# Performance work log

Hardware: AMD Instinct MI355X
Metric: run time of the kernel (lower is better)

## Reference

```python
import jax, jax.numpy as jnp
import numpy as np

NS = 16384  # number of samples
N = 2048    # number of sites


def setup_inputs() -> dict:
    key = jax.random.key(0)
    kx, kk = jax.random.split(key)
    x = jax.random.normal(kx, (NS, N), dtype=jnp.float32)
    kernel = 0.01 * jax.random.normal(kk, (N * (N - 1) // 2,), dtype=jnp.float32)
    return {"x": x, "kernel": kernel, "n": 4}


def reference(x, kernel, n):
    # Build strictly lower-triangular W from the kernel vector (sorted, unique indices)
    Nloc = x.shape[-1]
    il = jnp.tril_indices(Nloc, k=-1)
    W = jnp.zeros((Nloc, Nloc), dtype=kernel.dtype).at[il].set(
        kernel, unique_indices=True, indices_are_sorted=True)
    # z_nj = sum_i x_ni W_ji  ==  x @ W.T
    z = x @ W.T
    # each step: z_nk = sum_j z_nj W_kj x_nj  ==  (z * x) @ W.T
    z = jax.lax.fori_loop(0, n - 2, lambda i, zz: (zz * x) @ W.T, z)
    # logpsi_n = sum_l z_nl x_nl
    return jnp.sum(z * x, axis=-1)
```

## Files before the change

### kernel.cpp

```cpp
#include <hip/hip_runtime.h>
#include <stdint.h>

#define NSAMP 16384
#define NSITE 2048
#define BM 128
#define BN 128
#define BK 32
#define NT_M (NSAMP / BM)
#define NT_N (NSITE / BN)

typedef _Float16 f16x8 __attribute__((ext_vector_type(8)));
typedef float f32x16 __attribute__((ext_vector_type(16)));

__device__ __forceinline__ unsigned short f2h(float f) {
  _Float16 h = (_Float16)f;
  return __builtin_bit_cast(unsigned short, h);
}

__device__ __forceinline__ void gload_lds16(const void* g, void* l) {
  __builtin_amdgcn_global_load_lds(
      (const __attribute__((address_space(1))) void*)g,
      (__attribute__((address_space(3))) void*)l, 16, 0, 0);
}

#define SBAR() __builtin_amdgcn_sched_barrier(0)
#define BAR()  do { SBAR(); __builtin_amdgcn_s_barrier(); SBAR(); } while (0)
#define WLGKM(N) do { asm volatile("s_waitcnt lgkmcnt(" #N ")" ::: "memory"); SBAR(); } while (0)
#define WVM(N)   do { asm volatile("s_waitcnt vmcnt(" #N ")" ::: "memory"); SBAR(); } while (0)

__global__ void build_w_kernel(const float* __restrict__ kern,
                               unsigned short* __restrict__ W) {
  int idx = blockIdx.x * blockDim.x + threadIdx.x;
  int j = idx >> 11;
  int i = idx & (NSITE - 1);
  float v = 0.0f;
  if (i < j) v = kern[j * (j - 1) / 2 + i];
  W[idx] = f2h(v);
}

__global__ void build_x_kernel(const float* __restrict__ x,
                               unsigned short* __restrict__ X) {
  int idx = blockIdx.x * blockDim.x + threadIdx.x;
  const float4 v = reinterpret_cast<const float4*>(x)[idx];
  reinterpret_cast<ushort4*>(X)[idx] =
      make_ushort4(f2h(v.x), f2h(v.y), f2h(v.z), f2h(v.w));
}

template <int EPI>
__global__ __launch_bounds__(256, 3) void gemm_pass(
    const unsigned short* __restrict__ A, const unsigned short* __restrict__ W,
    const float* __restrict__ x, unsigned short* __restrict__ P,
    float* __restrict__ out) {
  __shared__ unsigned short lds[3][2][BM * BK];

  const int bid = blockIdx.x;
  const int g = bid >> 7;
  const int nt = (g & 1) ? (g >> 1) : (15 - (g >> 1));
  const int mt = bid & 127;
  const int m0 = mt * BM;
  const int n0 = nt * BN;

  const int tid = threadIdx.x;
  const int lane = tid & 63;
  const int wid = tid >> 6;
  const int wm = wid >> 1;
  const int wn = wid & 1;
  const int l32 = lane & 31;
  const int hi2 = lane >> 5;

  f32x16 acc[2][2] = {};
  f16x8 fa[2][2], fb[2][2];

  const int nkt = (n0 + BN) / BK;

  auto STAGE = [&](int kidx) {
    const int slot = kidx % 3;
#pragma unroll
    for (int inst = 0; inst < 4; ++inst) {
      const int p = inst >> 1;
      const int r = (inst & 1) * 64 + (tid >> 2);
      const int gch = (tid & 3) ^ ((r >> 1) & 3);
      const unsigned short* gp = p ? W : A;
      const int rb = p ? n0 : m0;
      const char* src =
          (const char*)(gp + (size_t)(rb + r) * NSITE + kidx * BK) + gch * 16;
      char* dst = (char*)&lds[slot][p][0] + (inst & 1) * 4096 + tid * 16;
      gload_lds16(src, dst);
    }
  };

  auto LDA_ = [&](int kh, int slot) {
#pragma unroll
    for (int mb = 0; mb < 2; ++mb) {
      const int row = wm * 64 + mb * 32 + l32;
      const int byte = row * 64 + ((((kh << 1) | hi2) ^ ((l32 >> 1) & 3)) << 4);
      fa[kh][mb] = *(const f16x8*)((const char*)&lds[slot][0][0] + byte);
    }
  };
  auto LDB_ = [&](int kh, int slot) {
#pragma unroll
    for (int nb = 0; nb < 2; ++nb) {
      const int row = wn * 64 + nb * 32 + l32;
      const int byte = row * 64 + ((((kh << 1) | hi2) ^ ((l32 >> 1) & 3)) << 4);
      fb[kh][nb] = *(const f16x8*)((const char*)&lds[slot][1][0] + byte);
    }
  };
  auto MM = [&](int kh) {
#pragma unroll
    for (int mb = 0; mb < 2; ++mb)
#pragma unroll
      for (int nb = 0; nb < 2; ++nb)
        acc[mb][nb] = __builtin_amdgcn_mfma_f32_32x32x16_f16(fa[kh][mb], fb[kh][nb],
                                                             acc[mb][nb], 0, 0, 0);
  };

  STAGE(0);
  STAGE(1);
  WVM(4);
  BAR();

  for (int t = 0; t < nkt; ++t) {
    const int slot = t % 3;
    LDB_(0, slot);
    LDA_(0, slot);
    if (t + 2 < nkt) STAGE(t + 2);
    LDA_(1, slot);
    LDB_(1, slot);
    WLGKM(4);
    __builtin_amdgcn_s_setprio(1);
    MM(0);
    WLGKM(0);
    MM(1);
    __builtin_amdgcn_s_setprio(0);
    if (t + 1 < nkt) {
      if (t + 2 < nkt) { WVM(4); } else { WVM(0); }
      BAR();
    }
  }

  if (EPI == 0) {
#pragma unroll
    for (int mb = 0; mb < 2; ++mb)
#pragma unroll
      for (int nb = 0; nb < 2; ++nb)
#pragma unroll
        for (int reg = 0; reg < 16; ++reg) {
          const int row = (reg & 3) + 8 * (reg >> 2) + 4 * hi2;
          const int grow = m0 + wm * 64 + mb * 32 + row;
          const int gcol = n0 + wn * 64 + nb * 32 + l32;
          const size_t off = (size_t)grow * NSITE + gcol;
          P[off] = f2h(acc[mb][nb][reg] * x[off]);
        }
  } else {
#pragma unroll
    for (int mb = 0; mb < 2; ++mb)
#pragma unroll
      for (int reg = 0; reg < 16; ++reg) {
        const int row = (reg & 3) + 8 * (reg >> 2) + 4 * hi2;
        const int grow = m0 + wm * 64 + mb * 32 + row;
        const int gcol0 = n0 + wn * 64 + l32;
        float s = acc[mb][0][reg] * x[(size_t)grow * NSITE + gcol0] +
                  acc[mb][1][reg] * x[(size_t)grow * NSITE + gcol0 + 32];
        s += __shfl_xor(s, 1);
        s += __shfl_xor(s, 2);
        s += __shfl_xor(s, 4);
        s += __shfl_xor(s, 8);
        s += __shfl_xor(s, 16);
        if (l32 == 0) atomicAdd(&out[grow], s);
      }
  }
}

extern "C" void kernel_launch(void* const* d_in, const int* in_sizes, int n_in,
                              void* d_out, int out_size, void* d_ws, size_t ws_size,
                              hipStream_t stream) {
  const float* x = (const float*)d_in[0];
  const float* kern = (const float*)d_in[1];
  float* out = (float*)d_out;

  unsigned short* W  = (unsigned short*)d_ws;
  unsigned short* X  = W + (size_t)NSITE * NSITE;
  unsigned short* P1 = X + (size_t)NSAMP * NSITE;
  unsigned short* P2 = P1 + (size_t)NSAMP * NSITE;

  hipMemsetAsync(d_out, 0, (size_t)NSAMP * sizeof(float), stream);
  build_w_kernel<<<(NSITE * NSITE) / 256, 256, 0, stream>>>(kern, W);
  build_x_kernel<<<(NSAMP * NSITE / 4) / 256, 256, 0, stream>>>(x, X);

  gemm_pass<0><<<NT_M * NT_N, 256, 0, stream>>>(X, W, x, P1, nullptr);
  gemm_pass<0><<<NT_M * NT_N, 256, 0, stream>>>(P1, W, x, P2, nullptr);
  gemm_pass<1><<<NT_M * NT_N, 256, 0, stream>>>(P2, W, x, nullptr, out);
}
```

Before: 417.0 us.

## Widen GEMM tile to 128x256 with 8 waves and fragment-ordered LDS staging

Doubles the N tile to 256 and runs 512-thread blocks with 8 waves in a 2x4 arrangement. Each staged K-slice of A and W now goes to LDS already in MFMA fragment order, so every wave reads contiguous 16-byte chunks without XOR swizzling. Blocks are reordered so the longest triangular N tiles are scheduled first. The epilogue reads the fp16 copy of x instead of the fp32 input to halve epilogue traffic, at some cost in accuracy. More data reuse per block comes with higher LDS use per block and fewer blocks per CU.

Measured after the change: 408.3 us. -2.1%, faster.

```diff
diff --git a/kernel.cpp b/kernel.cpp
--- a/kernel.cpp
+++ b/kernel.cpp
@@ -4,7 +4,7 @@
 #define NSAMP 16384
 #define NSITE 2048
 #define BM 128
-#define BN 128
+#define BN 256
 #define BK 32
 #define NT_M (NSAMP / BM)
 #define NT_N (NSITE / BN)
@@ -15,6 +15,9 @@
 __device__ __forceinline__ unsigned short f2h(float f) {
   _Float16 h = (_Float16)f;
   return __builtin_bit_cast(unsigned short, h);
+}
+__device__ __forceinline__ float h2f(unsigned short u) {
+  return (float)__builtin_bit_cast(_Float16, u);
 }
 
 __device__ __forceinline__ void gload_lds16(const void* g, void* l) {
@@ -47,15 +50,15 @@
 }
 
 template <int EPI>
-__global__ __launch_bounds__(256, 3) void gemm_pass(
+__global__ __launch_bounds__(512, 4) void gemm_pass(
     const unsigned short* __restrict__ A, const unsigned short* __restrict__ W,
-    const float* __restrict__ x, unsigned short* __restrict__ P,
+    const unsigned short* __restrict__ X, unsigned short* __restrict__ P,
     float* __restrict__ out) {
-  __shared__ unsigned short lds[3][2][BM * BK];
+  __shared__ unsigned short lds[3][12288];
 
   const int bid = blockIdx.x;
-  const int g = bid >> 7;
-  const int nt = (g & 1) ? (g >> 1) : (15 - (g >> 1));
+  const int g = (bid >> 7) & 3;
+  const int nt = (bid >> 9) ? (3 - g) : (7 - g);
   const int mt = bid & 127;
   const int m0 = mt * BM;
   const int n0 = nt * BN;
@@ -63,104 +66,92 @@
   const int tid = threadIdx.x;
   const int lane = tid & 63;
   const int wid = tid >> 6;
-  const int wm = wid >> 1;
-  const int wn = wid & 1;
+  const int wm = wid >> 2;
+  const int wn = wid & 3;
   const int l32 = lane & 31;
   const int hi2 = lane >> 5;
+  const int lbo = lane * 16;
 
   f32x16 acc[2][2] = {};
-  f16x8 fa[2][2], fb[2][2];
 
-  const int nkt = (n0 + BN) / BK;
+  const int nkt = 8 * (nt + 1);
 
-  auto STAGE = [&](int kidx) {
-    const int slot = kidx % 3;
-#pragma unroll
-    for (int inst = 0; inst < 4; ++inst) {
-      const int p = inst >> 1;
-      const int r = (inst & 1) * 64 + (tid >> 2);
-      const int gch = (tid & 3) ^ ((r >> 1) & 3);
-      const unsigned short* gp = p ? W : A;
-      const int rb = p ? n0 : m0;
-      const char* src =
-          (const char*)(gp + (size_t)(rb + r) * NSITE + kidx * BK) + gch * 16;
-      char* dst = (char*)&lds[slot][p][0] + (inst & 1) * 4096 + tid * 16;
-      gload_lds16(src, dst);
-    }
+  const int srow = ((tid >> 7) << 5) + (tid & 31);
+  const int skk = (((tid >> 6) & 1) << 4) + (((tid >> 5) & 1) << 3);
+  const unsigned short* sA = A + (size_t)(m0 + srow) * NSITE + skk;
+  const unsigned short* sB0 = W + (size_t)(n0 + srow) * NSITE + skk;
+  const unsigned short* sB1 = W + (size_t)(n0 + 128 + srow) * NSITE + skk;
+
+  auto STAGE = [&](int kidx, int slot) {
+    char* Ls = (char*)&lds[slot][0];
+    const int ko = kidx * BK;
+    gload_lds16(sA + ko, Ls + tid * 16);
+    gload_lds16(sB0 + ko, Ls + 8192 + tid * 16);
+    gload_lds16(sB1 + ko, Ls + 16384 + tid * 16);
   };
 
-  auto LDA_ = [&](int kh, int slot) {
-#pragma unroll
-    for (int mb = 0; mb < 2; ++mb) {
-      const int row = wm * 64 + mb * 32 + l32;
-      const int byte = row * 64 + ((((kh << 1) | hi2) ^ ((l32 >> 1) & 3)) << 4);
-      fa[kh][mb] = *(const f16x8*)((const char*)&lds[slot][0][0] + byte);
-    }
-  };
-  auto LDB_ = [&](int kh, int slot) {
-#pragma unroll
-    for (int nb = 0; nb < 2; ++nb) {
-      const int row = wn * 64 + nb * 32 + l32;
-      const int byte = row * 64 + ((((kh << 1) | hi2) ^ ((l32 >> 1) & 3)) << 4);
-      fb[kh][nb] = *(const f16x8*)((const char*)&lds[slot][1][0] + byte);
-    }
-  };
-  auto MM = [&](int kh) {
-#pragma unroll
-    for (int mb = 0; mb < 2; ++mb)
-#pragma unroll
-      for (int nb = 0; nb < 2; ++nb)
-        acc[mb][nb] = __builtin_amdgcn_mfma_f32_32x32x16_f16(fa[kh][mb], fb[kh][nb],
-                                                             acc[mb][nb], 0, 0, 0);
-  };
-
-  STAGE(0);
-  STAGE(1);
-  WVM(4);
+  STAGE(0, 0);
+  STAGE(1, 1);
+  WVM(3);
   BAR();
 
+  int slot = 0, slot2 = 2;
   for (int t = 0; t < nkt; ++t) {
-    const int slot = t % 3;
-    LDB_(0, slot);
-    LDA_(0, slot);
-    if (t + 2 < nkt) STAGE(t + 2);
-    LDA_(1, slot);
-    LDB_(1, slot);
+    const char* Ls = (const char*)&lds[slot][0];
+    f16x8 a0, a1, b0, b1, a2, a3, b2, b3;
+    a0 = *(const f16x8*)(Ls + (wm * 4 + 0) * 1024 + lbo);
+    a1 = *(const f16x8*)(Ls + (wm * 4 + 2) * 1024 + lbo);
+    b0 = *(const f16x8*)(Ls + 8192 + (wn * 4 + 0) * 1024 + lbo);
+    b1 = *(const f16x8*)(Ls + 8192 + (wn * 4 + 2) * 1024 + lbo);
+    SBAR();
+    a2 = *(const f16x8*)(Ls + (wm * 4 + 1) * 1024 + lbo);
+    a3 = *(const f16x8*)(Ls + (wm * 4 + 3) * 1024 + lbo);
+    b2 = *(const f16x8*)(Ls + 8192 + (wn * 4 + 1) * 1024 + lbo);
+    b3 = *(const f16x8*)(Ls + 8192 + (wn * 4 + 3) * 1024 + lbo);
+    SBAR();
+    if (t + 2 < nkt) STAGE(t + 2, slot2);
     WLGKM(4);
     __builtin_amdgcn_s_setprio(1);
-    MM(0);
+    acc[0][0] = __builtin_amdgcn_mfma_f32_32x32x16_f16(a0, b0, acc[0][0], 0, 0, 0);
+    acc[0][1] = __builtin_amdgcn_mfma_f32_32x32x16_f16(a0, b1, acc[0][1], 0, 0, 0);
+    acc[1][0] = __builtin_amdgcn_mfma_f32_32x32x16_f16(a1, b0, acc[1][0], 0, 0, 0);
+    acc[1][1] = __builtin_amdgcn_mfma_f32_32x32x16_f16(a1, b1, acc[1][1], 0, 0, 0);
     WLGKM(0);
-    MM(1);
+    acc[0][0] = __builtin_amdgcn_mfma_f32_32x32x16_f16(a2, b2, acc[0][0], 0, 0, 0);
+    acc[0][1] = __builtin_amdgcn_mfma_f32_32x32x16_f16(a2, b3, acc[0][1], 0, 0, 0);
+    acc[1][0] = __builtin_amdgcn_mfma_f32_32x32x16_f16(a3, b2, acc[1][0], 0, 0, 0);
+    acc[1][1] = __builtin_amdgcn_mfma_f32_32x32x16_f16(a3, b3, acc[1][1], 0, 0, 0);
     __builtin_amdgcn_s_setprio(0);
     if (t + 1 < nkt) {
-      if (t + 2 < nkt) { WVM(4); } else { WVM(0); }
+      if (t + 2 < nkt) { WVM(3); } else { WVM(0); }
       BAR();
     }
+    slot = (slot == 2) ? 0 : slot + 1;
+    slot2 = (slot2 == 2) ? 0 : slot2 + 1;
   }
 
   if (EPI == 0) {
 #pragma unroll
-    for (int mb = 0; mb < 2; ++mb)
+    for (int m = 0; m < 2; ++m)
 #pragma unroll
-      for (int nb = 0; nb < 2; ++nb)
+      for (int n = 0; n < 2; ++n)
 #pragma unroll
-        for (int reg = 0; reg < 16; ++reg) {
-          const int row = (reg & 3) + 8 * (reg >> 2) + 4 * hi2;
-          const int grow = m0 + wm * 64 + mb * 32 + row;
-          const int gcol = n0 + wn * 64 + nb * 32 + l32;
+        for (int r = 0; r < 16; ++r) {
+          const int row = (r & 3) + 8 * (r >> 2) + 4 * hi2;
+          const int grow = m0 + wm * 64 + m * 32 + row;
+          const int gcol = n0 + wn * 64 + n * 32 + l32;
           const size_t off = (size_t)grow * NSITE + gcol;
-          P[off] = f2h(acc[mb][nb][reg] * x[off]);
+          P[off] = f2h(acc[m][n][r] * h2f(X[off]));
         }
   } else {
 #pragma unroll
-    for (int mb = 0; mb < 2; ++mb)
+    for (int m = 0; m < 2; ++m)
 #pragma unroll
-      for (int reg = 0; reg < 16; ++reg) {
-        const int row = (reg & 3) + 8 * (reg >> 2) + 4 * hi2;
-        const int grow = m0 + wm * 64 + mb * 32 + row;
-        const int gcol0 = n0 + wn * 64 + l32;
-        float s = acc[mb][0][reg] * x[(size_t)grow * NSITE + gcol0] +
-                  acc[mb][1][reg] * x[(size_t)grow * NSITE + gcol0 + 32];
+      for (int r = 0; r < 16; ++r) {
+        const int row = (r & 3) + 8 * (r >> 2) + 4 * hi2;
+        const int grow = m0 + wm * 64 + m * 32 + row;
+        const size_t base = (size_t)grow * NSITE + n0 + wn * 64 + l32;
+        float s = acc[m][0][r] * h2f(X[base]) + acc[m][1][r] * h2f(X[base + 32]);
         s += __shfl_xor(s, 1);
         s += __shfl_xor(s, 2);
         s += __shfl_xor(s, 4);
@@ -187,7 +178,7 @@
   build_w_kernel<<<(NSITE * NSITE) / 256, 256, 0, stream>>>(kern, W);
   build_x_kernel<<<(NSAMP * NSITE / 4) / 256, 256, 0, stream>>>(x, X);
 
-  gemm_pass<0><<<NT_M * NT_N, 256, 0, stream>>>(X, W, x, P1, nullptr);
-  gemm_pass<0><<<NT_M * NT_N, 256, 0, stream>>>(P1, W, x, P2, nullptr);
-  gemm_pass<1><<<NT_M * NT_N, 256, 0, stream>>>(P2, W, x, nullptr, out);
+  gemm_pass<0><<<NT_M * NT_N, 512, 0, stream>>>(X, W, X, P1, nullptr);
+  gemm_pass<0><<<NT_M * NT_N, 512, 0, stream>>>(P1, W, X, P2, nullptr);
+  gemm_pass<1><<<NT_M * NT_N, 512, 0, stream>>>(P2, W, X, nullptr, out);
 }
```
